# Kernel tuning notes

Measured on AMD Instinct MI355X. Metric: run time of the kernel, lower is better.

The kernel has to match this reference:

```python
import jax, jax.numpy as jnp
import numpy as np

H = 128          # hidden size
D = 2048         # input size
B, T = 64, 256   # batch, seq_len


def _lstm_layer(x_proj, Whh, h0, c0):
    """x_proj: [B,T,4H] precomputed input projection (+ both biases).
    Returns (full hidden sequence [B,T,H], final hidden [B,H]).
    PyTorch gate order: i, f, g, o."""
    def step(carry, xt):
        h, c = carry
        g = xt + h @ Whh.T                      # [B,4H]
        i, f, gg, o = jnp.split(g, 4, axis=-1)
        i = jax.nn.sigmoid(i)
        f = jax.nn.sigmoid(f)
        gg = jnp.tanh(gg)
        o = jax.nn.sigmoid(o)
        c = f * c + i * gg
        h = o * jnp.tanh(c)
        return (h, c), h

    (hT, _), hs = jax.lax.scan(step, (h0, c0), jnp.swapaxes(x_proj, 0, 1))
    return jnp.swapaxes(hs, 0, 1), hT


def setup_inputs() -> dict:
    key = jax.random.key(0)
    ks = jax.random.split(key, 11)
    k = 1.0 / np.sqrt(H)  # torch default init bound
    u = lambda kk, shape: jax.random.uniform(kk, shape, jnp.float32, -k, k)
    return {
        "x":    jax.random.normal(ks[0], (B, T, D), jnp.float32),
        "Wih0": u(ks[1], (4 * H, D)),
        "Whh0": u(ks[2], (4 * H, H)),
        "bih0": u(ks[3], (4 * H,)),
        "bhh0": u(ks[4], (4 * H,)),
        "Wih1": u(ks[5], (4 * H, H)),
        "Whh1": u(ks[6], (4 * H, H)),
        "bih1": u(ks[7], (4 * H,)),
        "bhh1": u(ks[8], (4 * H,)),
        "Wfc":  u(ks[9], (1, H)),
        "bfc":  u(ks[10], (1,)),
    }


def reference(x, Wih0, Whh0, bih0, bhh0, Wih1, Whh1, bih1, bhh1, Wfc, bfc):
    b = x.shape[0]
    h0 = jnp.zeros((b, H), x.dtype)
    # layer 0: batch the big input GEMM across all timesteps
    xp0 = jnp.einsum('btd,gd->btg', x, Wih0) + bih0 + bhh0   # [B,T,4H]
    seq0, _ = _lstm_layer(xp0, Whh0, h0, h0)
    # layer 1 (dropout disabled in eval)
    xp1 = jnp.einsum('bth,gh->btg', seq0, Wih1) + bih1 + bhh1
    _, hT = _lstm_layer(xp1, Whh1, h0, h0)                   # h_n[-1]
    return hT @ Wfc.T + bfc                                  # [B,1]
```

## Files before the change

kernel.cpp:

```cpp
#include <hip/hip_runtime.h>
#include <math.h>

#define HH 128
#define DD 2048
#define BATCH 64
#define TT 256
#define G4 512
#define GB 16
#define HPAD 136

typedef __attribute__((ext_vector_type(8))) short bf16x8;
typedef __attribute__((ext_vector_type(4))) float f32x4;
typedef _Float16 f16x8 __attribute__((ext_vector_type(8)));


static __device__ __forceinline__ unsigned short f2bf_rne(float f) {
    union { float f; unsigned u; } v; v.f = f;
    unsigned r = v.u + 0x7fff + ((v.u >> 16) & 1);
    return (unsigned short)(r >> 16);
}
static __device__ __forceinline__ float bf2f(unsigned short b) {
    union { unsigned u; float f; } v; v.u = ((unsigned)b) << 16;
    return v.f;
}
static __device__ __forceinline__ float fexp2(float x) {
#if __has_builtin(__builtin_amdgcn_exp2f)
    return __builtin_amdgcn_exp2f(x);
#else
    return exp2f(x);
#endif
}
static __device__ __forceinline__ float frcp(float x) {
#if __has_builtin(__builtin_amdgcn_rcpf)
    return __builtin_amdgcn_rcpf(x);
#else
    return 1.f / x;
#endif
}
static __device__ __forceinline__ float sigmoid_f(float x) {
    return frcp(1.f + fexp2(-1.44269504f * x));
}
static __device__ __forceinline__ float tanh_f(float x) {
    float xx = fminf(fmaxf(x, -15.f), 15.f);
    float e = fexp2(2.88539008f * xx);
    return 1.f - 2.f * frcp(e + 1.f);
}

#define PK 40

__global__ __launch_bounds__(256) void gemm_split_bf16(
    const float* __restrict__ A, const float* __restrict__ Bw,
    const float* __restrict__ b1, const float* __restrict__ b2,
    float* __restrict__ C, int M, int N, int K)
{
    __shared__ unsigned short Ah[128 * PK], Al[128 * PK];
    __shared__ unsigned short Bh[128 * PK], Bl[128 * PK];

    const int tid = threadIdx.x;
    const int l = tid & 63;
    const int w = tid >> 6;
    const int wr = w >> 1, wc = w & 1;
    const int bm = blockIdx.y, bn = blockIdx.x;

    f32x4 acc[4][4];
#pragma unroll
    for (int m = 0; m < 4; ++m)
#pragma unroll
        for (int n = 0; n < 4; ++n) acc[m][n] = f32x4{0.f, 0.f, 0.f, 0.f};

    const float* Ab = A + (size_t)(bm * 128) * K;

    for (int k0 = 0; k0 < K; k0 += 32) {
        __syncthreads();
#pragma unroll
        for (int q = 0; q < 4; ++q) {
            int fid = tid + 256 * q;
            int r = fid >> 3;
            int kk = (fid & 7) << 2;
            int n = bn * 128 + r;
            int orign = ((n & 3) << 7) | (n >> 2);
            float4 av = *(const float4*)(Ab + (size_t)r * K + k0 + kk);
            float4 bv = *(const float4*)(Bw + (size_t)orign * K + k0 + kk);
            float a4[4] = {av.x, av.y, av.z, av.w};
            float b4[4] = {bv.x, bv.y, bv.z, bv.w};
            ushort4 ahv, alv, bhv, blv;
            unsigned short t;
            t = f2bf_rne(a4[0]); ahv.x = t; alv.x = f2bf_rne(a4[0] - bf2f(t));
            t = f2bf_rne(a4[1]); ahv.y = t; alv.y = f2bf_rne(a4[1] - bf2f(t));
            t = f2bf_rne(a4[2]); ahv.z = t; alv.z = f2bf_rne(a4[2] - bf2f(t));
            t = f2bf_rne(a4[3]); ahv.w = t; alv.w = f2bf_rne(a4[3] - bf2f(t));
            t = f2bf_rne(b4[0]); bhv.x = t; blv.x = f2bf_rne(b4[0] - bf2f(t));
            t = f2bf_rne(b4[1]); bhv.y = t; blv.y = f2bf_rne(b4[1] - bf2f(t));
            t = f2bf_rne(b4[2]); bhv.z = t; blv.z = f2bf_rne(b4[2] - bf2f(t));
            t = f2bf_rne(b4[3]); bhv.w = t; blv.w = f2bf_rne(b4[3] - bf2f(t));
            int off = r * PK + kk;
            *(ushort4*)&Ah[off] = ahv;
            *(ushort4*)&Al[off] = alv;
            *(ushort4*)&Bh[off] = bhv;
            *(ushort4*)&Bl[off] = blv;
        }
        __syncthreads();

        bf16x8 aH[4], aL[4], bH[4], bL[4];
#pragma unroll
        for (int m = 0; m < 4; ++m) {
            int row = wr * 64 + m * 16 + (l & 15);
            int off = row * PK + 8 * (l >> 4);
            aH[m] = *(const bf16x8*)&Ah[off];
            aL[m] = *(const bf16x8*)&Al[off];
        }
#pragma unroll
        for (int n = 0; n < 4; ++n) {
            int row = wc * 64 + n * 16 + (l & 15);
            int off = row * PK + 8 * (l >> 4);
            bH[n] = *(const bf16x8*)&Bh[off];
            bL[n] = *(const bf16x8*)&Bl[off];
        }
#pragma unroll
        for (int m = 0; m < 4; ++m)
#pragma unroll
            for (int n = 0; n < 4; ++n) {
                acc[m][n] = __builtin_amdgcn_mfma_f32_16x16x32_bf16(aH[m], bH[n], acc[m][n], 0, 0, 0);
                acc[m][n] = __builtin_amdgcn_mfma_f32_16x16x32_bf16(aH[m], bL[n], acc[m][n], 0, 0, 0);
                acc[m][n] = __builtin_amdgcn_mfma_f32_16x16x32_bf16(aL[m], bH[n], acc[m][n], 0, 0, 0);
            }
    }

#pragma unroll
    for (int n = 0; n < 4; ++n) {
        int cg = bn * 128 + wc * 64 + n * 16 + (l & 15);
        int orig = ((cg & 3) << 7) | (cg >> 2);
        float bias = b1[orig] + b2[orig];
        size_t cbase = (size_t)(cg >> 6) * 1024 + ((cg >> 4) & 3) * 256 + (cg & 15);
#pragma unroll
        for (int m = 0; m < 4; ++m) {
            int r0 = bm * 128 + wr * 64 + m * 16 + ((l >> 4) << 2);
            f32x4 v = acc[m][n];
#pragma unroll
            for (int i = 0; i < 4; ++i) {
                int r = r0 + i;
                int t = r & 255, b = r >> 8;
                C[(size_t)t * 32768 + (size_t)(b >> 4) * 8192 + cbase + (b & 15) * 16] = v[i] + bias;
            }
        }
    }
}

template <bool WRITE_SEQ, bool FINAL_FC>
__global__ __launch_bounds__(512, 1) void lstm_rec_mfma(
    const float* __restrict__ xp,
    const float* __restrict__ Whh,
    float* __restrict__ seq_out,
    const float* __restrict__ Wfc,
    const float* __restrict__ bfc,
    float* __restrict__ out)
{
    const int tid = threadIdx.x;
    const int l  = tid & 63;
    const int w  = tid >> 6;
    const int lb = l & 15;
    const int lg = l >> 4;
    const int blk = blockIdx.x;

    __shared__ ushort hbuf[2][GB][HPAD];
    __shared__ float red[8][GB];

    for (int i = tid; i < 2 * GB * HPAD; i += 512) ((ushort*)hbuf)[i] = 0;

    f16x8 wf[4][4];
#pragma unroll
    for (int mm = 0; mm < 4; ++mm) {
        int rp = (w * 4 + mm) * 16 + lb;
        int orig = ((rp & 3) << 7) | (rp >> 2);
        const float* wr_ = Whh + (size_t)orig * HH;
#pragma unroll
        for (int kt = 0; kt < 4; ++kt) {
            float4 x0 = *(const float4*)(wr_ + kt * 32 + lg * 8);
            float4 x1 = *(const float4*)(wr_ + kt * 32 + lg * 8 + 4);
            f16x8 f;
            f[0] = (_Float16)x0.x; f[1] = (_Float16)x0.y;
            f[2] = (_Float16)x0.z; f[3] = (_Float16)x0.w;
            f[4] = (_Float16)x1.x; f[5] = (_Float16)x1.y;
            f[6] = (_Float16)x1.z; f[7] = (_Float16)x1.w;
            wf[mm][kt] = f;
        }
    }

    const float* xbase = xp + (size_t)blk * 8192 + w * 1024 + lb * 16 + lg * 4;
    float4 X0[4], X1[4];
#pragma unroll
    for (int mm = 0; mm < 4; ++mm) X0[mm] = *(const float4*)(xbase + mm * 256);
#pragma unroll
    for (int mm = 0; mm < 4; ++mm) X1[mm] = *(const float4*)(xbase + 32768 + mm * 256);

    float c4[4] = {0.f, 0.f, 0.f, 0.f};
    float hv[4] = {0.f, 0.f, 0.f, 0.f};
    int cur = 0;
    __syncthreads();

    auto step = [&](int t, float4* X, int tp) {
        f16x8 bfr[4];
#pragma unroll
        for (int kt = 0; kt < 4; ++kt) {
            union { uint4 u; f16x8 h; } cvt;
            cvt.u = *(const uint4*)&hbuf[cur][lb][kt * 32 + lg * 8];
            bfr[kt] = cvt.h;
        }
        f32x4 acc[4];
#pragma unroll
        for (int mm = 0; mm < 4; ++mm)
            acc[mm] = f32x4{X[mm].x, X[mm].y, X[mm].z, X[mm].w};
        const float* pp = xbase + (size_t)tp * 32768;
#pragma unroll
        for (int mm = 0; mm < 4; ++mm) X[mm] = *(const float4*)(pp + mm * 256);

#pragma unroll
        for (int kt = 0; kt < 4; ++kt)
#pragma unroll
            for (int mm = 0; mm < 4; ++mm)
                acc[mm] = __builtin_amdgcn_mfma_f32_16x16x32_f16(wf[mm][kt], bfr[kt], acc[mm], 0, 0, 0);

#pragma unroll
        for (int mm = 0; mm < 4; ++mm) {
            float iv = sigmoid_f(acc[mm][0]);
            float fv = sigmoid_f(acc[mm][1]);
            float gg = tanh_f(acc[mm][2]);
            float ov = sigmoid_f(acc[mm][3]);
            float c = fmaf(fv, c4[mm], iv * gg);
            c4[mm] = c;
            float h = ov * tanh_f(c);
            hv[mm] = h;
            int u = (w * 4 + mm) * 4 + lg;
            union { _Float16 f; ushort s; } hc; hc.f = (_Float16)h;
            hbuf[cur ^ 1][lb][u] = hc.s;
            if (WRITE_SEQ)
                seq_out[((size_t)(blk * GB + lb) * TT + t) * HH + u] = h;
        }
        __syncthreads();
        cur ^= 1;
    };

    for (int t = 0; t < TT; t += 2) {
        int tp0 = (t + 2 < TT) ? t + 2 : TT - 1;
        int tp1 = (t + 3 < TT) ? t + 3 : TT - 1;
        step(t,     X0, tp0);
        step(t + 1, X1, tp1);
    }

    if (FINAL_FC) {
        float p = 0.f;
#pragma unroll
        for (int mm = 0; mm < 4; ++mm) {
            int u = (w * 4 + mm) * 4 + lg;
            p = fmaf(hv[mm], Wfc[u], p);
        }
        p += __shfl_xor(p, 16, 64);
        p += __shfl_xor(p, 32, 64);
        if (l < GB) red[w][l] = p;
        __syncthreads();
        if (tid < GB) {
            float s = bfc[0];
#pragma unroll
            for (int q = 0; q < 8; ++q) s += red[q][tid];
            out[blk * GB + tid] = s;
        }
    }
}

extern "C" void kernel_launch(void* const* d_in, const int* in_sizes, int n_in,
                              void* d_out, int out_size, void* d_ws, size_t ws_size,
                              hipStream_t stream)
{
    const float* x    = (const float*)d_in[0];
    const float* Wih0 = (const float*)d_in[1];
    const float* Whh0 = (const float*)d_in[2];
    const float* bih0 = (const float*)d_in[3];
    const float* bhh0 = (const float*)d_in[4];
    const float* Wih1 = (const float*)d_in[5];
    const float* Whh1 = (const float*)d_in[6];
    const float* bih1 = (const float*)d_in[7];
    const float* bhh1 = (const float*)d_in[8];
    const float* Wfc  = (const float*)d_in[9];
    const float* bfc  = (const float*)d_in[10];
    float* out = (float*)d_out;

    const int M = BATCH * TT;
    float* xp  = (float*)d_ws;
    float* seq = xp + (size_t)M * G4;

    gemm_split_bf16<<<dim3(G4 / 128, M / 128), 256, 0, stream>>>(
        x, Wih0, bih0, bhh0, xp, M, G4, DD);

    lstm_rec_mfma<true, false><<<BATCH / GB, 512, 0, stream>>>(
        xp, Whh0, seq, nullptr, nullptr, nullptr);

    gemm_split_bf16<<<dim3(G4 / 128, M / 128), 256, 0, stream>>>(
        seq, Wih1, bih1, bhh1, xp, M, G4, HH);

    lstm_rec_mfma<false, true><<<BATCH / GB, 512, 0, stream>>>(
        xp, Whh1, nullptr, Wfc, bfc, out);
}
```

Before: 868.6 us.

## Fuse both LSTM layers into one wavefront-pipelined recurrent kernel

Replaces the layer-0 recurrence, the layer-1 input GEMM and the layer-1 recurrence with a single kernel. Layer 0 runs one timestep ahead of layer 1 inside the same loop, and layer 1's input projection is computed on the fly from layer 0's hidden state held in LDS. This drops the sequence write and readback, one GEMM launch and one recurrent launch, and halves the number of serial barrier-bound step loops. In exchange, each step does more MFMA work and register pressure triples because three weight matrices are kept in registers, which could cause spills.

After: 902.0 us. 1.04x slower.

```diff
diff --git a/kernel.cpp b/kernel.cpp
--- a/kernel.cpp
+++ b/kernel.cpp
@@ -146,11 +146,21 @@
     }
 }
 
-template <bool WRITE_SEQ, bool FINAL_FC>
-__global__ __launch_bounds__(512, 1) void lstm_rec_mfma(
+__global__ void prep_bias1(const float* __restrict__ bih1,
+                           const float* __restrict__ bhh1,
+                           float* __restrict__ bias1p)
+{
+    int n = threadIdx.x;
+    int orig = ((n & 3) << 7) | (n >> 2);
+    bias1p[n] = bih1[orig] + bhh1[orig];
+}
+
+__global__ __launch_bounds__(512) void lstm_fused(
     const float* __restrict__ xp,
-    const float* __restrict__ Whh,
-    float* __restrict__ seq_out,
+    const float* __restrict__ Whh0,
+    const float* __restrict__ Wih1,
+    const float* __restrict__ Whh1,
+    const float* __restrict__ bias1p,
     const float* __restrict__ Wfc,
     const float* __restrict__ bfc,
     float* __restrict__ out)
@@ -162,108 +172,146 @@
     const int lg = l >> 4;
     const int blk = blockIdx.x;
 
-    __shared__ ushort hbuf[2][GB][HPAD];
+    __shared__ ushort h0b[2][GB][HPAD];
+    __shared__ ushort h1b[2][GB][HPAD];
     __shared__ float red[8][GB];
 
-    for (int i = tid; i < 2 * GB * HPAD; i += 512) ((ushort*)hbuf)[i] = 0;
-
-    f16x8 wf[4][4];
+    for (int i = tid; i < 2 * GB * HPAD; i += 512) {
+        ((ushort*)h0b)[i] = 0;
+        ((ushort*)h1b)[i] = 0;
+    }
+
+    f16x8 wf0[4][4], wi1[4][4], wh1[4][4];
 #pragma unroll
     for (int mm = 0; mm < 4; ++mm) {
         int rp = (w * 4 + mm) * 16 + lb;
         int orig = ((rp & 3) << 7) | (rp >> 2);
-        const float* wr_ = Whh + (size_t)orig * HH;
 #pragma unroll
         for (int kt = 0; kt < 4; ++kt) {
-            float4 x0 = *(const float4*)(wr_ + kt * 32 + lg * 8);
-            float4 x1 = *(const float4*)(wr_ + kt * 32 + lg * 8 + 4);
+            const float* p0 = Whh0 + (size_t)orig * HH + kt * 32 + lg * 8;
+            const float* p1 = Wih1 + (size_t)orig * HH + kt * 32 + lg * 8;
+            const float* p2 = Whh1 + (size_t)orig * HH + kt * 32 + lg * 8;
+            float4 a0 = *(const float4*)p0, a1 = *(const float4*)(p0 + 4);
+            float4 b0 = *(const float4*)p1, b1v = *(const float4*)(p1 + 4);
+            float4 c0v = *(const float4*)p2, c1v = *(const float4*)(p2 + 4);
             f16x8 f;
-            f[0] = (_Float16)x0.x; f[1] = (_Float16)x0.y;
-            f[2] = (_Float16)x0.z; f[3] = (_Float16)x0.w;
-            f[4] = (_Float16)x1.x; f[5] = (_Float16)x1.y;
-            f[6] = (_Float16)x1.z; f[7] = (_Float16)x1.w;
-            wf[mm][kt] = f;
+            f[0]=(_Float16)a0.x; f[1]=(_Float16)a0.y; f[2]=(_Float16)a0.z; f[3]=(_Float16)a0.w;
+            f[4]=(_Float16)a1.x; f[5]=(_Float16)a1.y; f[6]=(_Float16)a1.z; f[7]=(_Float16)a1.w;
+            wf0[mm][kt] = f;
+            f[0]=(_Float16)b0.x; f[1]=(_Float16)b0.y; f[2]=(_Float16)b0.z; f[3]=(_Float16)b0.w;
+            f[4]=(_Float16)b1v.x; f[5]=(_Float16)b1v.y; f[6]=(_Float16)b1v.z; f[7]=(_Float16)b1v.w;
+            wi1[mm][kt] = f;
+            f[0]=(_Float16)c0v.x; f[1]=(_Float16)c0v.y; f[2]=(_Float16)c0v.z; f[3]=(_Float16)c0v.w;
+            f[4]=(_Float16)c1v.x; f[5]=(_Float16)c1v.y; f[6]=(_Float16)c1v.z; f[7]=(_Float16)c1v.w;
+            wh1[mm][kt] = f;
         }
     }
 
     const float* xbase = xp + (size_t)blk * 8192 + w * 1024 + lb * 16 + lg * 4;
-    float4 X0[4], X1[4];
-#pragma unroll
-    for (int mm = 0; mm < 4; ++mm) X0[mm] = *(const float4*)(xbase + mm * 256);
-#pragma unroll
-    for (int mm = 0; mm < 4; ++mm) X1[mm] = *(const float4*)(xbase + 32768 + mm * 256);
-
-    float c4[4] = {0.f, 0.f, 0.f, 0.f};
-    float hv[4] = {0.f, 0.f, 0.f, 0.f};
-    int cur = 0;
+    const int ubase = w * 16 + lg;
+
+    f32x4 X[4];
+#pragma unroll
+    for (int mm = 0; mm < 4; ++mm) X[mm] = *(const f32x4*)(xbase + mm * 256);
+
+    float c0[4] = {0.f,0.f,0.f,0.f}, c1[4] = {0.f,0.f,0.f,0.f}, hv[4];
     __syncthreads();
 
-    auto step = [&](int t, float4* X, int tp) {
-        f16x8 bfr[4];
+#pragma unroll
+    for (int mm = 0; mm < 4; ++mm) {
+        float iv = sigmoid_f(X[mm][0]);
+        float fv = sigmoid_f(X[mm][1]);
+        float gg = tanh_f(X[mm][2]);
+        float ov = sigmoid_f(X[mm][3]);
+        float c = fmaf(fv, 0.f, iv * gg);
+        c0[mm] = c;
+        float h = ov * tanh_f(c);
+        union { _Float16 f; ushort s; } hc; hc.f = (_Float16)h;
+        h0b[0][lb][ubase + mm * 4] = hc.s;
+    }
+#pragma unroll
+    for (int mm = 0; mm < 4; ++mm)
+        X[mm] = *(const f32x4*)(xbase + 32768 + mm * 256);
+    __syncthreads();
+
+    for (int p = 0; p < TT; ++p) {
+        const int rb = p & 1, wb = rb ^ 1;
+
+        f32x4 a0[4], a1[4];
+#pragma unroll
+        for (int mm = 0; mm < 4; ++mm) a0[mm] = X[mm];
+#pragma unroll
+        for (int mm = 0; mm < 4; ++mm)
+            a1[mm] = *(const f32x4*)(bias1p + (w * 4 + mm) * 16 + lg * 4);
+
 #pragma unroll
         for (int kt = 0; kt < 4; ++kt) {
             union { uint4 u; f16x8 h; } cvt;
-            cvt.u = *(const uint4*)&hbuf[cur][lb][kt * 32 + lg * 8];
-            bfr[kt] = cvt.h;
-        }
-        f32x4 acc[4];
+            cvt.u = *(const uint4*)&h0b[rb][lb][kt * 32 + lg * 8];
+            f16x8 bh = cvt.h;
+#pragma unroll
+            for (int mm = 0; mm < 4; ++mm)
+                a0[mm] = __builtin_amdgcn_mfma_f32_16x16x32_f16(wf0[mm][kt], bh, a0[mm], 0, 0, 0);
+#pragma unroll
+            for (int mm = 0; mm < 4; ++mm)
+                a1[mm] = __builtin_amdgcn_mfma_f32_16x16x32_f16(wi1[mm][kt], bh, a1[mm], 0, 0, 0);
+        }
+#pragma unroll
+        for (int kt = 0; kt < 4; ++kt) {
+            union { uint4 u; f16x8 h; } cvt;
+            cvt.u = *(const uint4*)&h1b[rb][lb][kt * 32 + lg * 8];
+            f16x8 bh = cvt.h;
+#pragma unroll
+            for (int mm = 0; mm < 4; ++mm)
+                a1[mm] = __builtin_amdgcn_mfma_f32_16x16x32_f16(wh1[mm][kt], bh, a1[mm], 0, 0, 0);
+        }
+
+        int tn = (p + 2 < TT) ? p + 2 : TT - 1;
 #pragma unroll
         for (int mm = 0; mm < 4; ++mm)
-            acc[mm] = f32x4{X[mm].x, X[mm].y, X[mm].z, X[mm].w};
-        const float* pp = xbase + (size_t)tp * 32768;
-#pragma unroll
-        for (int mm = 0; mm < 4; ++mm) X[mm] = *(const float4*)(pp + mm * 256);
-
-#pragma unroll
-        for (int kt = 0; kt < 4; ++kt)
-#pragma unroll
-            for (int mm = 0; mm < 4; ++mm)
-                acc[mm] = __builtin_amdgcn_mfma_f32_16x16x32_f16(wf[mm][kt], bfr[kt], acc[mm], 0, 0, 0);
+            X[mm] = *(const f32x4*)(xbase + (size_t)tn * 32768 + mm * 256);
 
 #pragma unroll
         for (int mm = 0; mm < 4; ++mm) {
-            float iv = sigmoid_f(acc[mm][0]);
-            float fv = sigmoid_f(acc[mm][1]);
-            float gg = tanh_f(acc[mm][2]);
-            float ov = sigmoid_f(acc[mm][3]);
-            float c = fmaf(fv, c4[mm], iv * gg);
-            c4[mm] = c;
+            float iv = sigmoid_f(a0[mm][0]);
+            float fv = sigmoid_f(a0[mm][1]);
+            float gg = tanh_f(a0[mm][2]);
+            float ov = sigmoid_f(a0[mm][3]);
+            float c = fmaf(fv, c0[mm], iv * gg);
+            c0[mm] = c;
+            float h = ov * tanh_f(c);
+            union { _Float16 f; ushort s; } hc; hc.f = (_Float16)h;
+            h0b[wb][lb][ubase + mm * 4] = hc.s;
+        }
+#pragma unroll
+        for (int mm = 0; mm < 4; ++mm) {
+            float iv = sigmoid_f(a1[mm][0]);
+            float fv = sigmoid_f(a1[mm][1]);
+            float gg = tanh_f(a1[mm][2]);
+            float ov = sigmoid_f(a1[mm][3]);
+            float c = fmaf(fv, c1[mm], iv * gg);
+            c1[mm] = c;
             float h = ov * tanh_f(c);
             hv[mm] = h;
-            int u = (w * 4 + mm) * 4 + lg;
             union { _Float16 f; ushort s; } hc; hc.f = (_Float16)h;
-            hbuf[cur ^ 1][lb][u] = hc.s;
-            if (WRITE_SEQ)
-                seq_out[((size_t)(blk * GB + lb) * TT + t) * HH + u] = h;
+            h1b[wb][lb][ubase + mm * 4] = hc.s;
         }
         __syncthreads();
-        cur ^= 1;
-    };
-
-    for (int t = 0; t < TT; t += 2) {
-        int tp0 = (t + 2 < TT) ? t + 2 : TT - 1;
-        int tp1 = (t + 3 < TT) ? t + 3 : TT - 1;
-        step(t,     X0, tp0);
-        step(t + 1, X1, tp1);
-    }
-
-    if (FINAL_FC) {
-        float p = 0.f;
-#pragma unroll
-        for (int mm = 0; mm < 4; ++mm) {
-            int u = (w * 4 + mm) * 4 + lg;
-            p = fmaf(hv[mm], Wfc[u], p);
-        }
-        p += __shfl_xor(p, 16, 64);
-        p += __shfl_xor(p, 32, 64);
-        if (l < GB) red[w][l] = p;
-        __syncthreads();
-        if (tid < GB) {
-            float s = bfc[0];
-#pragma unroll
-            for (int q = 0; q < 8; ++q) s += red[q][tid];
-            out[blk * GB + tid] = s;
-        }
+    }
+
+    float pr = 0.f;
+#pragma unroll
+    for (int mm = 0; mm < 4; ++mm)
+        pr = fmaf(hv[mm], Wfc[ubase + mm * 4], pr);
+    pr += __shfl_xor(pr, 16, 64);
+    pr += __shfl_xor(pr, 32, 64);
+    if (l < GB) red[w][l] = pr;
+    __syncthreads();
+    if (tid < GB) {
+        float s = bfc[0];
+#pragma unroll
+        for (int q = 0; q < 8; ++q) s += red[q][tid];
+        out[blk * GB + tid] = s;
     }
 }
 
@@ -285,18 +333,14 @@
     float* out = (float*)d_out;
 
     const int M = BATCH * TT;
-    float* xp  = (float*)d_ws;
-    float* seq = xp + (size_t)M * G4;
+    float* xp      = (float*)d_ws;
+    float* bias1p  = xp + (size_t)M * G4;
 
     gemm_split_bf16<<<dim3(G4 / 128, M / 128), 256, 0, stream>>>(
         x, Wih0, bih0, bhh0, xp, M, G4, DD);
 
-    lstm_rec_mfma<true, false><<<BATCH / GB, 512, 0, stream>>>(
-        xp, Whh0, seq, nullptr, nullptr, nullptr);
-
-    gemm_split_bf16<<<dim3(G4 / 128, M / 128), 256, 0, stream>>>(
-        seq, Wih1, bih1, bhh1, xp, M, G4, HH);
-
-    lstm_rec_mfma<false, true><<<BATCH / GB, 512, 0, stream>>>(
-        xp, Whh1, nullptr, Wfc, bfc, out);
-}
+    prep_bias1<<<1, G4, 0, stream>>>(bih1, bhh1, bias1p);
+
+    lstm_fused<<<BATCH / GB, 512, 0, stream>>>(
+        xp, Whh0, Wih1, Whh1, bias1p, Wfc, bfc, out);
+}
```
